# Kernel optimization log

Hardware: AMD Instinct MI355X
Metric: run time of the kernel (lower is better)

## Reference

```python
import jax, jax.numpy as jnp
import numpy as np

T, LQ, C = 6, 300, 256
NH, NL, PC, TW, PT = 8, 4, 4, 2, 2
DFF = 1024
HD = C // NH
SHAPES = [(96, 128), (48, 64), (24, 32), (12, 16)]
LIN = sum(h * w for h, w in SHAPES)
EPS = 1e-5


def _ln(x, g, b):
    m = x.mean(-1, keepdims=True)
    v = ((x - m) ** 2).mean(-1, keepdims=True)
    return (x - m) * jax.lax.rsqrt(v + EPS) * g + b


def _bilinear(img, loc):
    # img [T, Hl, Wl, NH, HD]; loc [T, Q, NH, P, 2] (x, y), normalized [0,1],
    # grid_sample align_corners=False + zero padding convention.
    Hl, Wl = img.shape[1], img.shape[2]
    x = loc[..., 0] * Wl - 0.5
    y = loc[..., 1] * Hl - 0.5
    x0f = jnp.floor(x)
    y0f = jnp.floor(y)
    wx = x - x0f
    wy = y - y0f
    x0 = x0f.astype(jnp.int32)
    y0 = y0f.astype(jnp.int32)
    flat = img.transpose(0, 3, 1, 2, 4).reshape(img.shape[0], NH, Hl * Wl, HD)
    b = jnp.arange(img.shape[0])[:, None, None, None]
    h = jnp.arange(NH)[None, :, None, None]

    def corner(yi, xi, w):
        valid = (xi >= 0) & (xi < Wl) & (yi >= 0) & (yi < Hl)
        idx = jnp.clip(yi, 0, Hl - 1) * Wl + jnp.clip(xi, 0, Wl - 1)
        g = flat[b, h, idx.transpose(0, 2, 1, 3)]  # [T, NH, Q, P, HD]
        w = jnp.where(valid, w, 0.0).transpose(0, 2, 1, 3)
        return g * w[..., None]

    out = (corner(y0, x0, (1 - wx) * (1 - wy)) + corner(y0, x0 + 1, wx * (1 - wy))
           + corner(y0 + 1, x0, (1 - wx) * wy) + corner(y0 + 1, x0 + 1, wx * wy))
    return out.transpose(0, 2, 1, 3, 4)  # [T, Q, NH, P, HD]


def _forward(tgt, query_pos, reference_points, curr_frame_offsets,
             other_frames_temporal_offsets, src, src_padding_mask,
             in_proj_w, in_proj_b, sa_out_w, sa_out_b,
             norm1_g, norm1_b, norm2_g, norm2_b, norm3_g, norm3_b,
             value_w, value_b, soff_w, soff_b, toff_w, toff_b,
             attn_w, attn_b, cross_out_w, cross_out_b,
             lin1_w, lin1_b, lin2_w, lin2_b):
    # ---- self attention (per-frame MHA over queries) ----
    q = tgt + query_pos
    wq, wk, wv = jnp.split(in_proj_w, 3, axis=0)
    bq, bk, bv = jnp.split(in_proj_b, 3)
    qh = ((q @ wq.T + bq) * (1.0 / np.sqrt(HD))).reshape(T, LQ, NH, HD)
    kh = (q @ wk.T + bk).reshape(T, LQ, NH, HD)
    vh = (tgt @ wv.T + bv).reshape(T, LQ, NH, HD)
    att = jax.nn.softmax(jnp.einsum('bqhd,bkhd->bhqk', qh, kh), axis=-1)
    sa = jnp.einsum('bhqk,bkhd->bqhd', att, vh).reshape(T, LQ, C) @ sa_out_w.T + sa_out_b
    tgt = _ln(tgt + sa, norm2_g, norm2_b)

    # ---- temporal multi-scale deformable cross attention ----
    qc = tgt + query_pos
    value = src @ value_w.T + value_b
    value = jnp.where(src_padding_mask[..., None], 0.0, value)
    value = value.reshape(T, LIN, NH, HD)

    soff = (qc @ soff_w.T + soff_b).reshape(T, LQ, NH, NL, PC, 2)
    toff = (qc @ toff_w.T + toff_b).reshape(T, LQ, NH, NL, TW, PT, 2)
    aw = (qc @ attn_w.T + attn_b).reshape(T, LQ, NH, NL * (PC + TW * PT))
    aw = jax.nn.softmax(aw, axis=-1).reshape(T, LQ, NH, NL, PC + TW * PT)
    aw_c = aw[..., :PC]                                  # [T,LQ,NH,NL,PC]
    aw_t = aw[..., PC:].reshape(T, LQ, NH, NL, TW, PT)

    norm = jnp.array([[w, h] for h, w in SHAPES], jnp.float32)  # [NL,2] (x,y)
    ref = reference_points[:, :, None, :, None, :]       # [T,LQ,1,NL,1,2]
    cfo = curr_frame_offsets[:, :, None, :, None, :]
    loc_c = ref + cfo + soff / norm[None, None, None, :, None, :]
    ofo = other_frames_temporal_offsets.transpose(0, 1, 3, 2, 4)[:, :, None, :, :, None, :]
    loc_t = ref[:, :, :, :, None, :, :] + ofo + toff / norm[None, None, None, :, None, None, :]

    # temporal window frame indices: nearest neighbours, clipped to clip bounds
    deltas = np.array([-(i // 2 + 1) if i % 2 == 0 else (i // 2 + 1) for i in range(TW)])
    frame_idx = np.clip(np.arange(T)[:, None] + deltas[None, :], 0, T - 1)  # [T,TW]

    out = jnp.zeros((T, LQ, NH, HD), tgt.dtype)
    start = 0
    for l, (hl, wl) in enumerate(SHAPES):
        v_l = value[:, start:start + hl * wl].reshape(T, hl, wl, NH, HD)
        s = _bilinear(v_l, loc_c[:, :, :, l])            # [T,LQ,NH,PC,HD]
        out = out + (s * aw_c[:, :, :, l, :, None]).sum(3)
        for w in range(TW):
            s = _bilinear(v_l[frame_idx[:, w]], loc_t[:, :, :, l, w])
            out = out + (s * aw_t[:, :, :, l, w, :, None]).sum(3)
        start += hl * wl
    cross = out.reshape(T, LQ, C) @ cross_out_w.T + cross_out_b
    tgt = _ln(tgt + cross, norm1_g, norm1_b)

    # ---- FFN ----
    ff = jax.nn.relu(tgt @ lin1_w.T + lin1_b) @ lin2_w.T + lin2_b
    return _ln(tgt + ff, norm3_g, norm3_b)


def setup_inputs():
    ks = jax.random.split(jax.random.key(0), 24)
    r = lambda i, s: jax.random.normal(ks[i], s, jnp.float32)
    u = lambda i, s: jax.random.uniform(ks[i], s, dtype=jnp.float32)
    w = lambda i, s: r(i, s) * 0.02
    shp = np.array(SHAPES, np.int64)
    lsi = np.concatenate([[0], np.cumsum(shp[:, 0] * shp[:, 1])[:-1]])
    return {
        'tgt': r(0, (T, LQ, C)),
        'query_pos': r(1, (T, LQ, C)),
        'reference_points': u(2, (T, LQ, NL, 2)),
        'curr_frame_offsets': u(3, (T, LQ, NL, 2)) * 0.1,
        'other_frames_temporal_offsets': u(4, (T, LQ, TW, NL, 2)) * 0.1,
        'src': r(5, (T, LIN, C)),
        'src_spatial_shapes': jnp.asarray(shp),
        'level_start_index': jnp.asarray(lsi),
        'src_padding_mask': jnp.zeros((T, LIN), bool),
        'in_proj_w': w(6, (3 * C, C)), 'in_proj_b': jnp.zeros((3 * C,)),
        'sa_out_w': w(7, (C, C)), 'sa_out_b': jnp.zeros((C,)),
        'norm1_g': jnp.ones((C,)), 'norm1_b': jnp.zeros((C,)),
        'norm2_g': jnp.ones((C,)), 'norm2_b': jnp.zeros((C,)),
        'norm3_g': jnp.ones((C,)), 'norm3_b': jnp.zeros((C,)),
        'value_w': w(8, (C, C)), 'value_b': jnp.zeros((C,)),
        'soff_w': w(9, (NH * NL * PC * 2, C)), 'soff_b': jnp.zeros((NH * NL * PC * 2,)),
        'toff_w': w(10, (NH * NL * TW * PT * 2, C)), 'toff_b': jnp.zeros((NH * NL * TW * PT * 2,)),
        'attn_w': w(11, (NH * NL * (PC + TW * PT), C)), 'attn_b': jnp.zeros((NH * NL * (PC + TW * PT),)),
        'cross_out_w': w(12, (C, C)), 'cross_out_b': jnp.zeros((C,)),
        'lin1_w': w(13, (DFF, C)), 'lin1_b': jnp.zeros((DFF,)),
        'lin2_w': w(14, (C, DFF)), 'lin2_b': jnp.zeros((C,)),
    }


def reference(tgt, query_pos, reference_points, curr_frame_offsets,
              other_frames_temporal_offsets, src, src_spatial_shapes,
              level_start_index, src_padding_mask,
              in_proj_w, in_proj_b, sa_out_w, sa_out_b,
              norm1_g, norm1_b, norm2_g, norm2_b, norm3_g, norm3_b,
              value_w, value_b, soff_w, soff_b, toff_w, toff_b,
              attn_w, attn_b, cross_out_w, cross_out_b,
              lin1_w, lin1_b, lin2_w, lin2_b):
    # src_spatial_shapes / level_start_index are static (match SHAPES constants)
    return _forward(tgt, query_pos, reference_points, curr_frame_offsets,
                    other_frames_temporal_offsets, src, src_padding_mask,
                    in_proj_w, in_proj_b, sa_out_w, sa_out_b,
                    norm1_g, norm1_b, norm2_g, norm2_b, norm3_g, norm3_b,
                    value_w, value_b, soff_w, soff_b, toff_w, toff_b,
                    attn_w, attn_b, cross_out_w, cross_out_b,
                    lin1_w, lin1_b, lin2_w, lin2_b)
```

## Files before the change

### kernel.cpp

```cpp
#include <hip/hip_runtime.h>
#include <math.h>

#define T_ 6
#define LQ_ 300
#define C_ 256
#define NH_ 8
#define HD_ 32
#define NL_ 4
#define PC_ 4
#define TW_ 2
#define PT_ 2
#define DFF_ 1024
#define LIN_ 16320
#define NQ_ (T_*LQ_)

typedef unsigned int uint32;
typedef unsigned short us;

__device__ __forceinline__ float b2f(us u) {
    union { float f; unsigned i; } x; x.i = ((unsigned)u) << 16; return x.f;
}
__device__ __forceinline__ us f2b(float f) {
    union { float f; unsigned i; } x; x.f = f;
    unsigned r = x.i + 0x7fffu + ((x.i >> 16) & 1u);
    return (us)(r >> 16);
}
__device__ __forceinline__ uint32 pack2(float a, float b) {
    return (uint32)f2b(a) | ((uint32)f2b(b) << 16);
}

typedef __bf16 bf16x8 __attribute__((ext_vector_type(8)));
typedef float  f32x4  __attribute__((ext_vector_type(4)));

__global__ void add_f32(const float4* __restrict__ a, const float4* __restrict__ b,
                        float4* __restrict__ o, int n4) {
    int i = blockIdx.x * 256 + threadIdx.x;
    if (i < n4) {
        float4 x = a[i], y = b[i];
        o[i] = make_float4(x.x + y.x, x.y + y.y, x.z + y.z, x.w + y.w);
    }
}

template<bool RELU>
__device__ __forceinline__ void gemm64_core(
        us* As, us* Bs,
        const float* __restrict__ A, const float* __restrict__ Bw,
        const float* __restrict__ bias, float* __restrict__ Cmat,
        int ldc, int cn0, int M, int K) {
    constexpr int LDA = 40;
    int tid  = threadIdx.x;
    int wave = tid >> 6, lane = tid & 63;
    int bm = blockIdx.x * 64;
    int wm = (wave >> 1) * 32, wn = (wave & 1) * 32;

    f32x4 acc00 = {0.f,0.f,0.f,0.f}, acc01 = {0.f,0.f,0.f,0.f};
    f32x4 acc10 = {0.f,0.f,0.f,0.f}, acc11 = {0.f,0.f,0.f,0.f};

    int srow = tid >> 2, scol = (tid & 3) * 8;
    int arow = bm + srow;
    const bool aval = arow < M;
    const size_t aoff = (size_t)arow * K + scol;
    const size_t boff = (size_t)srow * K + scol;

    int fr = lane & 15, quad = lane >> 4;
    const us* pa0 = As + (wm + fr) * LDA + quad * 8;
    const us* pa1 = pa0 + 16 * LDA;
    const us* pb0 = Bs + (wn + fr) * LDA + quad * 8;
    const us* pb1 = pb0 + 16 * LDA;

    for (int k0 = 0; k0 < K; k0 += 256) {
        float4 ar[8][2], br[8][2];
        #pragma unroll
        for (int c = 0; c < 8; ++c) {
            int kk = k0 + c * 32;
            if (aval) {
                ar[c][0] = *(const float4*)(A + aoff + kk);
                ar[c][1] = *(const float4*)(A + aoff + kk + 4);
            } else {
                ar[c][0] = make_float4(0.f,0.f,0.f,0.f);
                ar[c][1] = make_float4(0.f,0.f,0.f,0.f);
            }
            br[c][0] = *(const float4*)(Bw + boff + kk);
            br[c][1] = *(const float4*)(Bw + boff + kk + 4);
        }
        #pragma unroll
        for (int c = 0; c < 8; ++c) {
            uint4 ap, bp;
            ap.x = pack2(ar[c][0].x, ar[c][0].y); ap.y = pack2(ar[c][0].z, ar[c][0].w);
            ap.z = pack2(ar[c][1].x, ar[c][1].y); ap.w = pack2(ar[c][1].z, ar[c][1].w);
            bp.x = pack2(br[c][0].x, br[c][0].y); bp.y = pack2(br[c][0].z, br[c][0].w);
            bp.z = pack2(br[c][1].x, br[c][1].y); bp.w = pack2(br[c][1].z, br[c][1].w);
            __syncthreads();
            *(uint4*)(As + srow * LDA + scol) = ap;
            *(uint4*)(Bs + srow * LDA + scol) = bp;
            __syncthreads();
            bf16x8 a0 = *(const bf16x8*)pa0;
            bf16x8 a1 = *(const bf16x8*)pa1;
            bf16x8 b0 = *(const bf16x8*)pb0;
            bf16x8 b1 = *(const bf16x8*)pb1;
            acc00 = __builtin_amdgcn_mfma_f32_16x16x32_bf16(a0, b0, acc00, 0, 0, 0);
            acc01 = __builtin_amdgcn_mfma_f32_16x16x32_bf16(a0, b1, acc01, 0, 0, 0);
            acc10 = __builtin_amdgcn_mfma_f32_16x16x32_bf16(a1, b0, acc10, 0, 0, 0);
            acc11 = __builtin_amdgcn_mfma_f32_16x16x32_bf16(a1, b1, acc11, 0, 0, 0);
        }
    }

    int n0l = wn + fr, n1l = n0l + 16;
    float bias0 = bias[n0l], bias1 = bias[n1l];
    int mbase = bm + wm + quad * 4;
    #pragma unroll
    for (int r = 0; r < 4; ++r) {
        int m0 = mbase + r, m1 = m0 + 16;
        float v00 = acc00[r] + bias0, v01 = acc01[r] + bias1;
        float v10 = acc10[r] + bias0, v11 = acc11[r] + bias1;
        if (RELU) {
            v00 = fmaxf(v00, 0.f); v01 = fmaxf(v01, 0.f);
            v10 = fmaxf(v10, 0.f); v11 = fmaxf(v11, 0.f);
        }
        if (m0 < M) {
            Cmat[(size_t)m0 * ldc + cn0 + n0l] = v00;
            Cmat[(size_t)m0 * ldc + cn0 + n1l] = v01;
        }
        if (m1 < M) {
            Cmat[(size_t)m1 * ldc + cn0 + n0l] = v10;
            Cmat[(size_t)m1 * ldc + cn0 + n1l] = v11;
        }
    }
}

template<bool RELU>
__global__ __launch_bounds__(256, 2) void gemm_std(
        const float* __restrict__ A, const float* __restrict__ W,
        const float* __restrict__ bias, float* __restrict__ C,
        int M, int N, int K) {
    __shared__ __align__(16) us As[64 * 40];
    __shared__ __align__(16) us Bs[64 * 40];
    int cn0 = blockIdx.y * 64;
    gemm64_core<RELU>(As, Bs, A, W + (size_t)cn0 * K, bias + cn0, C, N, cn0, M, K);
}

__global__ __launch_bounds__(256, 2) void gemm_qkv(
        const float* __restrict__ qin, const float* __restrict__ tgt,
        const float* __restrict__ w, const float* __restrict__ b,
        float* __restrict__ qkb, float* __restrict__ vbuf) {
    __shared__ __align__(16) us As[64 * 40];
    __shared__ __align__(16) us Bs[64 * 40];
    int y = blockIdx.y;
    const float* A; const float* W; const float* bias; float* O; int ldc, cn0;
    if (y < 8) {
        A = qin; W = w + (size_t)y * 64 * 256; bias = b + y * 64;
        O = qkb; ldc = 512; cn0 = y * 64;
    } else {
        int yy = y - 8;
        A = tgt; W = w + (size_t)(512 + yy * 64) * 256; bias = b + 512 + yy * 64;
        O = vbuf; ldc = 256; cn0 = yy * 64;
    }
    gemm64_core<false>(As, Bs, A, W, bias, O, ldc, cn0, NQ_, 256);
}

__global__ __launch_bounds__(256, 2) void gemm_proj3(
        const float* __restrict__ qc,
        const float* __restrict__ sw, const float* __restrict__ sb,
        const float* __restrict__ tw, const float* __restrict__ tb,
        const float* __restrict__ aw, const float* __restrict__ ab,
        float* __restrict__ so, float* __restrict__ to, float* __restrict__ ao) {
    __shared__ __align__(16) us As[64 * 40];
    __shared__ __align__(16) us Bs[64 * 40];
    int y = blockIdx.y, g = y >> 2, cn0 = (y & 3) * 64;
    const float* W; const float* bias; float* O;
    if (g == 0)      { W = sw; bias = sb; O = so; }
    else if (g == 1) { W = tw; bias = tb; O = to; }
    else             { W = aw; bias = ab; O = ao; }
    gemm64_core<false>(As, Bs, qc, W + (size_t)cn0 * 256, bias + cn0, O, 256, cn0, NQ_, 256);
}

__global__ __launch_bounds__(256, 2) void gemm_value(
        const float* __restrict__ src, const float* __restrict__ W,
        const float* __restrict__ bias, us* __restrict__ out) {
    constexpr int LDA = 40;
    __shared__ __align__(16) us As[64 * LDA];
    __shared__ __align__(16) us Bs[256 * LDA];
    int tid = threadIdx.x, wave = tid >> 6, lane = tid & 63;
    int bm = blockIdx.x * 64;
    int fr = lane & 15, quad = lane >> 4;
    f32x4 acc[4][4];
    #pragma unroll
    for (int i = 0; i < 4; ++i)
        #pragma unroll
        for (int j = 0; j < 4; ++j) { f32x4 z = {0.f,0.f,0.f,0.f}; acc[i][j] = z; }

    for (int k0 = 0; k0 < 256; k0 += 32) {
        float4 av[2], bv[8];
        #pragma unroll
        for (int i = 0; i < 2; ++i) {
            int f = i * 256 + tid;
            av[i] = *(const float4*)(src + (size_t)(bm + (f >> 3)) * 256 + k0 + (f & 7) * 4);
        }
        #pragma unroll
        for (int i = 0; i < 8; ++i) {
            int f = i * 256 + tid;
            bv[i] = *(const float4*)(W + (size_t)(f >> 3) * 256 + k0 + (f & 7) * 4);
        }
        __syncthreads();
        #pragma unroll
        for (int i = 0; i < 2; ++i) {
            int f = i * 256 + tid;
            uint2 p; p.x = pack2(av[i].x, av[i].y); p.y = pack2(av[i].z, av[i].w);
            *(uint2*)(As + (f >> 3) * LDA + (f & 7) * 4) = p;
        }
        #pragma unroll
        for (int i = 0; i < 8; ++i) {
            int f = i * 256 + tid;
            uint2 p; p.x = pack2(bv[i].x, bv[i].y); p.y = pack2(bv[i].z, bv[i].w);
            *(uint2*)(Bs + (f >> 3) * LDA + (f & 7) * 4) = p;
        }
        __syncthreads();
        bf16x8 af[4], bfv[4];
        #pragma unroll
        for (int mt = 0; mt < 4; ++mt)
            af[mt] = *(const bf16x8*)(As + (mt * 16 + fr) * LDA + quad * 8);
        #pragma unroll
        for (int nt = 0; nt < 4; ++nt)
            bfv[nt] = *(const bf16x8*)(Bs + (wave * 64 + nt * 16 + fr) * LDA + quad * 8);
        #pragma unroll
        for (int mt = 0; mt < 4; ++mt)
            #pragma unroll
            for (int nt = 0; nt < 4; ++nt)
                acc[mt][nt] = __builtin_amdgcn_mfma_f32_16x16x32_bf16(af[mt], bfv[nt], acc[mt][nt], 0, 0, 0);
    }
    #pragma unroll
    for (int nt = 0; nt < 4; ++nt) {
        int n = wave * 64 + nt * 16 + fr;
        float bs = bias[n];
        #pragma unroll
        for (int mt = 0; mt < 4; ++mt) {
            int mbase = bm + mt * 16 + quad * 4;
            #pragma unroll
            for (int r = 0; r < 4; ++r)
                out[(size_t)(mbase + r) * 256 + n] = f2b(acc[mt][nt][r] + bs);
        }
    }
}

__global__ __launch_bounds__(256) void attn_kernel(
        const float* __restrict__ qk, const float* __restrict__ vb,
        float* __restrict__ sain) {
    __shared__ uint32 Ksu[300 * 17];
    __shared__ uint32 Vsu[300 * 17];
    __shared__ float  Qs[32 * 32];
    __shared__ float  ps[4][304];
    int t = blockIdx.x / NH_, h = blockIdx.x % NH_;
    int q0 = blockIdx.y * 32;
    int tid = threadIdx.x;

    for (int idx = tid; idx < 300 * 16; idx += 256) {
        int row = idx >> 4, cc = idx & 15;
        float2 kv = *(const float2*)(qk + (size_t)(t * 300 + row) * 512 + 256 + h * 32 + 2 * cc);
        float2 vv = *(const float2*)(vb + (size_t)(t * 300 + row) * 256 + h * 32 + 2 * cc);
        Ksu[row * 17 + cc] = pack2(kv.x, kv.y);
        Vsu[row * 17 + cc] = pack2(vv.x, vv.y);
    }
    for (int idx = tid; idx < 1024; idx += 256) {
        int row = idx >> 5, d = idx & 31;
        int q = q0 + row;
        Qs[idx] = (q < 300) ? qk[(size_t)(t * 300 + q) * 512 + h * 32 + d] : 0.f;
    }
    __syncthreads();

    int wavei = tid >> 6, lane = tid & 63;
    const float scale = 0.17677669529663687f;

    for (int i = 0; i < 8; ++i) {
        int q = q0 + wavei * 8 + i;
        int ql = wavei * 8 + i;
        float qv[32];
        #pragma unroll
        for (int d = 0; d < 32; ++d) qv[d] = Qs[ql * 32 + d];

        float sc[5], mx = -1e30f;
        #pragma unroll
        for (int m = 0; m < 5; ++m) {
            int k = lane + 64 * m;
            float s = -1e30f;
            if (k < 300) {
                s = 0.f;
                #pragma unroll
                for (int dd = 0; dd < 16; ++dd) {
                    uint32 u = Ksu[k * 17 + dd];
                    s += qv[2 * dd]     * b2f((us)u)
                       + qv[2 * dd + 1] * b2f((us)(u >> 16));
                }
                s *= scale;
            }
            sc[m] = s; mx = fmaxf(mx, s);
        }
        #pragma unroll
        for (int off = 1; off < 64; off <<= 1) mx = fmaxf(mx, __shfl_xor(mx, off));
        float sum = 0.f;
        #pragma unroll
        for (int m = 0; m < 5; ++m) {
            int k = lane + 64 * m;
            float ev = (k < 300) ? __expf(sc[m] - mx) : 0.f;
            if (k < 300) ps[wavei][k] = ev;
            sum += ev;
        }
        #pragma unroll
        for (int off = 1; off < 64; off <<= 1) sum += __shfl_xor(sum, off);
        float inv = 1.f / sum;
        __syncthreads();

        int e16 = lane & 15, kh = lane >> 4;
        float ox = 0.f, oy = 0.f;
        int kbeg = kh * 75;
        for (int k = kbeg; k < kbeg + 75; ++k) {
            float p = ps[wavei][k];
            uint32 u = Vsu[k * 17 + e16];
            ox += p * b2f((us)u);
            oy += p * b2f((us)(u >> 16));
        }
        ox += __shfl_xor(ox, 16); ox += __shfl_xor(ox, 32);
        oy += __shfl_xor(oy, 16); oy += __shfl_xor(oy, 32);
        if (q < 300 && kh == 0) {
            *(float2*)(sain + (size_t)(t * 300 + q) * 256 + h * 32 + 2 * e16)
                = make_float2(ox * inv, oy * inv);
        }
        __syncthreads();
    }
}

__global__ __launch_bounds__(256) void sample_kernel(
        const float* __restrict__ awl,   const float* __restrict__ refp,
        const float* __restrict__ cfo,   const float* __restrict__ ofo,
        const float* __restrict__ soffo, const float* __restrict__ toffo,
        const us* __restrict__ value, float* __restrict__ samp) {
    const int HL[4] = {96, 48, 24, 12};
    const int WL[4] = {128, 64, 32, 16};
    const int ST[4] = {0, 12288, 15360, 16128};
    int b = blockIdx.x;
    int t = b / LQ_;
    int tid = threadIdx.x, h = tid >> 5, d = tid & 31;
    size_t row = (size_t)b;

    float logit = awl[row * 256 + h * 32 + d];
    float mx = logit;
    #pragma unroll
    for (int off = 16; off >= 1; off >>= 1) mx = fmaxf(mx, __shfl_xor(mx, off, 32));
    float e = __expf(logit - mx);
    float s = e;
    #pragma unroll
    for (int off = 16; off >= 1; off >>= 1) s += __shfl_xor(s, off, 32);
    float myw = e / s;

    float acc = 0.f;
    for (int smp = 0; smp < 32; ++smp) {
        int l = smp >> 3, j = smp & 7;
        float wgt = __shfl(myw, smp, 32);
        int Hl = HL[l], Wl = WL[l], st = ST[l];
        float rx = refp[(row * 4 + l) * 2 + 0];
        float ry = refp[(row * 4 + l) * 2 + 1];
        float lx, ly; int frame;
        if (j < 4) {
            lx = rx + cfo[(row * 4 + l) * 2 + 0]
               + soffo[row * 256 + h * 32 + l * 8 + j * 2 + 0] / (float)Wl;
            ly = ry + cfo[(row * 4 + l) * 2 + 1]
               + soffo[row * 256 + h * 32 + l * 8 + j * 2 + 1] / (float)Hl;
            frame = t;
        } else {
            int wi = (j - 4) >> 1, p = (j - 4) & 1;
            lx = rx + ofo[((row * 2 + wi) * 4 + l) * 2 + 0]
               + toffo[row * 256 + h * 32 + l * 8 + wi * 4 + p * 2 + 0] / (float)Wl;
            ly = ry + ofo[((row * 2 + wi) * 4 + l) * 2 + 1]
               + toffo[row * 256 + h * 32 + l * 8 + wi * 4 + p * 2 + 1] / (float)Hl;
            frame = t + (wi == 0 ? -1 : 1);
            frame = frame < 0 ? 0 : (frame > T_ - 1 ? T_ - 1 : frame);
        }
        float x = lx * (float)Wl - 0.5f, y = ly * (float)Hl - 0.5f;
        float xf = floorf(x), yf = floorf(y);
        float wx = x - xf, wy = y - yf;
        int x0 = (int)xf, y0 = (int)yf;
        float sacc = 0.f;
        size_t base = ((size_t)frame * LIN_ + st) * 256 + h * 32 + d;
        #pragma unroll
        for (int cy = 0; cy < 2; ++cy) {
            int yi = y0 + cy;
            if (yi < 0 || yi >= Hl) continue;
            float wyv = cy ? wy : 1.f - wy;
            #pragma unroll
            for (int cx = 0; cx < 2; ++cx) {
                int xi = x0 + cx;
                if (xi < 0 || xi >= Wl) continue;
                float wv = wyv * (cx ? wx : 1.f - wx);
                sacc += wv * b2f(value[base + (size_t)(yi * Wl + xi) * 256]);
            }
        }
        acc += wgt * sacc;
    }
    samp[row * 256 + h * 32 + d] = acc;
}

__global__ __launch_bounds__(256) void ln_kernel(
        const float* __restrict__ x, const float* __restrict__ y,
        const float* __restrict__ g, const float* __restrict__ bb,
        float* __restrict__ out,
        const float* __restrict__ pos, float* __restrict__ out2) {
    int row = blockIdx.x, c = threadIdx.x;
    size_t idx = (size_t)row * 256 + c;
    float v = x[idx] + y[idx];
    float s = v;
    #pragma unroll
    for (int off = 1; off < 64; off <<= 1) s += __shfl_xor(s, off);
    __shared__ float red[4];
    int wv = c >> 6;
    if ((c & 63) == 0) red[wv] = s;
    __syncthreads();
    float mean = (red[0] + red[1] + red[2] + red[3]) * (1.0f / 256.0f);
    float dv = v - mean;
    float s2 = dv * dv;
    #pragma unroll
    for (int off = 1; off < 64; off <<= 1) s2 += __shfl_xor(s2, off);
    __syncthreads();
    if ((c & 63) == 0) red[wv] = s2;
    __syncthreads();
    float var = (red[0] + red[1] + red[2] + red[3]) * (1.0f / 256.0f);
    float o = dv * rsqrtf(var + 1e-5f) * g[c] + bb[c];
    out[idx] = o;
    if (out2) out2[idx] = o + pos[idx];
}

extern "C" void kernel_launch(void* const* d_in, const int* in_sizes, int n_in,
                              void* d_out, int out_size, void* d_ws, size_t ws_size,
                              hipStream_t stream) {
    (void)in_sizes; (void)n_in; (void)out_size; (void)ws_size;
    typedef const float* cfp;
    cfp tgt   = (cfp)d_in[0];
    cfp qpos  = (cfp)d_in[1];
    cfp refp  = (cfp)d_in[2];
    cfp cfo   = (cfp)d_in[3];
    cfp ofo   = (cfp)d_in[4];
    cfp src   = (cfp)d_in[5];
    cfp in_proj_w = (cfp)d_in[9];
    cfp in_proj_b = (cfp)d_in[10];
    cfp sa_out_w  = (cfp)d_in[11];
    cfp sa_out_b  = (cfp)d_in[12];
    cfp n1g = (cfp)d_in[13], n1b = (cfp)d_in[14];
    cfp n2g = (cfp)d_in[15], n2b = (cfp)d_in[16];
    cfp n3g = (cfp)d_in[17], n3b = (cfp)d_in[18];
    cfp value_w = (cfp)d_in[19], value_b = (cfp)d_in[20];
    cfp soff_w = (cfp)d_in[21], soff_b = (cfp)d_in[22];
    cfp toff_w = (cfp)d_in[23], toff_b = (cfp)d_in[24];
    cfp attn_w = (cfp)d_in[25], attn_b = (cfp)d_in[26];
    cfp cross_w = (cfp)d_in[27], cross_b = (cfp)d_in[28];
    cfp lin1_w = (cfp)d_in[29], lin1_b = (cfp)d_in[30];
    cfp lin2_w = (cfp)d_in[31], lin2_b = (cfp)d_in[32];

    char* wp = (char*)d_ws;
    const size_t ROWB = (size_t)NQ_ * 256 * 4;
    us* value = (us*)wp;  wp += (size_t)T_ * LIN_ * 256 * 2;
    float* bigreg = (float*)wp;  wp += 4 * ROWB;
    float* qin  = bigreg;
    float* qkb  = bigreg + (size_t)NQ_ * 256;
    float* vbuf = bigreg + (size_t)NQ_ * 768;
    float* ff1  = bigreg;
    float* sain   = (float*)wp; wp += ROWB;   float* awl    = sain;
    float* sap    = (float*)wp; wp += ROWB;   float* soffo  = sap;
    float* tgt2   = (float*)wp; wp += ROWB;   float* ff2    = tgt2;
    float* qc     = (float*)wp; wp += ROWB;   float* samp   = qc;
    float* toffo  = (float*)wp; wp += ROWB;
    float* crossp = (float*)wp; wp += ROWB;
    float* tgt3   = (float*)wp; wp += ROWB;

    dim3 blk(256);
    const int mb = (NQ_ + 63) / 64;

    add_f32<<<dim3((NQ_ * 64 + 255) / 256), blk, 0, stream>>>(
        (const float4*)tgt, (const float4*)qpos, (float4*)qin, NQ_ * 64);
    gemm_qkv<<<dim3(mb, 12), blk, 0, stream>>>(qin, tgt, in_proj_w, in_proj_b, qkb, vbuf);
    attn_kernel<<<dim3(T_ * NH_, 10), blk, 0, stream>>>(qkb, vbuf, sain);
    gemm_std<false><<<dim3(mb, 4), blk, 0, stream>>>(sain, sa_out_w, sa_out_b, sap, NQ_, 256, 256);
    ln_kernel<<<dim3(NQ_), blk, 0, stream>>>(tgt, sap, n2g, n2b, tgt2, qpos, qc);
    gemm_proj3<<<dim3(mb, 12), blk, 0, stream>>>(qc, soff_w, soff_b, toff_w, toff_b,
                                                 attn_w, attn_b, soffo, toffo, awl);
    gemm_value<<<dim3((T_ * LIN_) / 64), blk, 0, stream>>>(src, value_w, value_b, value);
    sample_kernel<<<dim3(NQ_), blk, 0, stream>>>(awl, refp, cfo, ofo, soffo, toffo, value, samp);
    gemm_std<false><<<dim3(mb, 4), blk, 0, stream>>>(samp, cross_w, cross_b, crossp, NQ_, 256, 256);
    ln_kernel<<<dim3(NQ_), blk, 0, stream>>>(tgt2, crossp, n1g, n1b, tgt3, nullptr, nullptr);
    gemm_std<true><<<dim3(mb, 16), blk, 0, stream>>>(tgt3, lin1_w, lin1_b, ff1, NQ_, 1024, 256);
    gemm_std<false><<<dim3(mb, 4), blk, 0, stream>>>(ff1, lin2_w, lin2_b, ff2, NQ_, 256, 1024);
    ln_kernel<<<dim3(NQ_), blk, 0, stream>>>(tgt3, ff2, n3g, n3b, (float*)d_out, nullptr, nullptr);
}
```

Baseline: 404.9 us.

## Fuse residual+LayerNorm into full-width GEMMs and fold pos-add into QKV GEMM

Replaces the three out-projection GEMM + separate LayerNorm kernel pairs with one full-row (N=256) GEMM kernel that adds bias and residual, computes mean/variance per row via shuffles and shared memory, and writes the normalized output. It also folds the tgt+query_pos addition into the QKV GEMM's A-load, and adds register prefetching of the next K chunk in the full GEMM. The value GEMM moves first and pack2 uses the hardware bf16 conversion. This removes several launches and intermediate round trips. The cost is fewer blocks (mb=29 only) for the fused GEMMs, lower parallelism, and single-pass variance with slightly different numerics.

```diff
diff --git a/kernel.cpp b/kernel.cpp
--- a/kernel.cpp
+++ b/kernel.cpp
@@ -1,4 +1,5 @@
 #include <hip/hip_runtime.h>
+#include <hip/hip_bf16.h>
 #include <math.h>
 
 #define T_ 6
@@ -26,25 +27,19 @@
     return (us)(r >> 16);
 }
 __device__ __forceinline__ uint32 pack2(float a, float b) {
-    return (uint32)f2b(a) | ((uint32)f2b(b) << 16);
+    union { __hip_bfloat162 h; uint32 u; } c;
+    c.h = __float22bfloat162_rn(make_float2(a, b));
+    return c.u;
 }
 
 typedef __bf16 bf16x8 __attribute__((ext_vector_type(8)));
 typedef float  f32x4  __attribute__((ext_vector_type(4)));
-
-__global__ void add_f32(const float4* __restrict__ a, const float4* __restrict__ b,
-                        float4* __restrict__ o, int n4) {
-    int i = blockIdx.x * 256 + threadIdx.x;
-    if (i < n4) {
-        float4 x = a[i], y = b[i];
-        o[i] = make_float4(x.x + y.x, x.y + y.y, x.z + y.z, x.w + y.w);
-    }
-}
 
 template<bool RELU>
 __device__ __forceinline__ void gemm64_core(
         us* As, us* Bs,
-        const float* __restrict__ A, const float* __restrict__ Bw,
+        const float* __restrict__ A, const float* __restrict__ A2,
+        const float* __restrict__ Bw,
         const float* __restrict__ bias, float* __restrict__ Cmat,
         int ldc, int cn0, int M, int K) {
     constexpr int LDA = 40;
@@ -76,6 +71,12 @@
             if (aval) {
                 ar[c][0] = *(const float4*)(A + aoff + kk);
                 ar[c][1] = *(const float4*)(A + aoff + kk + 4);
+                if (A2) {
+                    float4 p0 = *(const float4*)(A2 + aoff + kk);
+                    float4 p1 = *(const float4*)(A2 + aoff + kk + 4);
+                    ar[c][0].x += p0.x; ar[c][0].y += p0.y; ar[c][0].z += p0.z; ar[c][0].w += p0.w;
+                    ar[c][1].x += p1.x; ar[c][1].y += p1.y; ar[c][1].z += p1.z; ar[c][1].w += p1.w;
+                }
             } else {
                 ar[c][0] = make_float4(0.f,0.f,0.f,0.f);
                 ar[c][1] = make_float4(0.f,0.f,0.f,0.f);
@@ -136,26 +137,24 @@
     __shared__ __align__(16) us As[64 * 40];
     __shared__ __align__(16) us Bs[64 * 40];
     int cn0 = blockIdx.y * 64;
-    gemm64_core<RELU>(As, Bs, A, W + (size_t)cn0 * K, bias + cn0, C, N, cn0, M, K);
+    gemm64_core<RELU>(As, Bs, A, nullptr, W + (size_t)cn0 * K, bias + cn0, C, N, cn0, M, K);
 }
 
 __global__ __launch_bounds__(256, 2) void gemm_qkv(
-        const float* __restrict__ qin, const float* __restrict__ tgt,
+        const float* __restrict__ tgt, const float* __restrict__ qpos,
         const float* __restrict__ w, const float* __restrict__ b,
         float* __restrict__ qkb, float* __restrict__ vbuf) {
     __shared__ __align__(16) us As[64 * 40];
     __shared__ __align__(16) us Bs[64 * 40];
     int y = blockIdx.y;
-    const float* A; const float* W; const float* bias; float* O; int ldc, cn0;
     if (y < 8) {
-        A = qin; W = w + (size_t)y * 64 * 256; bias = b + y * 64;
-        O = qkb; ldc = 512; cn0 = y * 64;
+        gemm64_core<false>(As, Bs, tgt, qpos, w + (size_t)y * 64 * 256, b + y * 64,
+                           qkb, 512, y * 64, NQ_, 256);
     } else {
         int yy = y - 8;
-        A = tgt; W = w + (size_t)(512 + yy * 64) * 256; bias = b + 512 + yy * 64;
-        O = vbuf; ldc = 256; cn0 = yy * 64;
-    }
-    gemm64_core<false>(As, Bs, A, W, bias, O, ldc, cn0, NQ_, 256);
+        gemm64_core<false>(As, Bs, tgt, nullptr, w + (size_t)(512 + yy * 64) * 256,
+                           b + 512 + yy * 64, vbuf, 256, yy * 64, NQ_, 256);
+    }
 }
 
 __global__ __launch_bounds__(256, 2) void gemm_proj3(
@@ -171,37 +170,57 @@
     if (g == 0)      { W = sw; bias = sb; O = so; }
     else if (g == 1) { W = tw; bias = tb; O = to; }
     else             { W = aw; bias = ab; O = ao; }
-    gemm64_core<false>(As, Bs, qc, W + (size_t)cn0 * 256, bias + cn0, O, 256, cn0, NQ_, 256);
-}
-
-__global__ __launch_bounds__(256, 2) void gemm_value(
-        const float* __restrict__ src, const float* __restrict__ W,
-        const float* __restrict__ bias, us* __restrict__ out) {
+    gemm64_core<false>(As, Bs, qc, nullptr, W + (size_t)cn0 * 256, bias + cn0, O, 256, cn0, NQ_, 256);
+}
+
+template<int MODE>
+__global__ __launch_bounds__(256, 2) void gemm_full(
+        const float* __restrict__ A, const float* __restrict__ W,
+        const float* __restrict__ bias, int M, int K,
+        us* __restrict__ out_bf,
+        const float* __restrict__ resid, const float* __restrict__ lng,
+        const float* __restrict__ lnb, float* __restrict__ out_ln,
+        const float* __restrict__ pos, float* __restrict__ out2) {
     constexpr int LDA = 40;
     __shared__ __align__(16) us As[64 * LDA];
     __shared__ __align__(16) us Bs[256 * LDA];
+    __shared__ float lred[2][64][4];
+    __shared__ float lmv[2][64];
     int tid = threadIdx.x, wave = tid >> 6, lane = tid & 63;
     int bm = blockIdx.x * 64;
     int fr = lane & 15, quad = lane >> 4;
+
     f32x4 acc[4][4];
     #pragma unroll
     for (int i = 0; i < 4; ++i)
         #pragma unroll
         for (int j = 0; j < 4; ++j) { f32x4 z = {0.f,0.f,0.f,0.f}; acc[i][j] = z; }
 
-    for (int k0 = 0; k0 < 256; k0 += 32) {
-        float4 av[2], bv[8];
+    const int KC = K >> 5;
+    float4 av[2], bv[8];
+
+    auto ldA = [&](int c) {
+        int k0 = c * 32;
         #pragma unroll
         for (int i = 0; i < 2; ++i) {
             int f = i * 256 + tid;
-            av[i] = *(const float4*)(src + (size_t)(bm + (f >> 3)) * 256 + k0 + (f & 7) * 4);
-        }
+            int r = bm + (f >> 3);
+            if (r < M) av[i] = *(const float4*)(A + (size_t)r * K + k0 + (f & 7) * 4);
+            else       av[i] = make_float4(0.f, 0.f, 0.f, 0.f);
+        }
+    };
+    auto ldB = [&](int c) {
+        int k0 = c * 32;
         #pragma unroll
         for (int i = 0; i < 8; ++i) {
             int f = i * 256 + tid;
-            bv[i] = *(const float4*)(W + (size_t)(f >> 3) * 256 + k0 + (f & 7) * 4);
-        }
-        __syncthreads();
+            bv[i] = *(const float4*)(W + (size_t)(f >> 3) * K + k0 + (f & 7) * 4);
+        }
+    };
+
+    ldA(0); ldB(0);
+    for (int c = 0; c < KC; ++c) {
+        if (c) __syncthreads();
         #pragma unroll
         for (int i = 0; i < 2; ++i) {
             int f = i * 256 + tid;
@@ -215,6 +234,7 @@
             *(uint2*)(Bs + (f >> 3) * LDA + (f & 7) * 4) = p;
         }
         __syncthreads();
+        if (c + 1 < KC) { ldA(c + 1); ldB(c + 1); }
         bf16x8 af[4], bfv[4];
         #pragma unroll
         for (int mt = 0; mt < 4; ++mt)
@@ -228,16 +248,88 @@
             for (int nt = 0; nt < 4; ++nt)
                 acc[mt][nt] = __builtin_amdgcn_mfma_f32_16x16x32_bf16(af[mt], bfv[nt], acc[mt][nt], 0, 0, 0);
     }
-    #pragma unroll
-    for (int nt = 0; nt < 4; ++nt) {
-        int n = wave * 64 + nt * 16 + fr;
-        float bs = bias[n];
+
+    if (MODE == 0) {
+        #pragma unroll
+        for (int nt = 0; nt < 4; ++nt) {
+            int n = wave * 64 + nt * 16 + fr;
+            float bs = bias[n];
+            #pragma unroll
+            for (int mt = 0; mt < 4; ++mt) {
+                int mbase = bm + mt * 16 + quad * 4;
+                #pragma unroll
+                for (int r = 0; r < 4; ++r) {
+                    int m = mbase + r;
+                    if (m < M) out_bf[(size_t)m * 256 + n] = f2b(acc[mt][nt][r] + bs);
+                }
+            }
+        }
+    } else {
+        int col[4]; float bcol[4];
+        #pragma unroll
+        for (int nt = 0; nt < 4; ++nt) {
+            col[nt] = wave * 64 + nt * 16 + fr;
+            bcol[nt] = bias[col[nt]];
+        }
         #pragma unroll
         for (int mt = 0; mt < 4; ++mt) {
-            int mbase = bm + mt * 16 + quad * 4;
             #pragma unroll
-            for (int r = 0; r < 4; ++r)
-                out[(size_t)(mbase + r) * 256 + n] = f2b(acc[mt][nt][r] + bs);
+            for (int r = 0; r < 4; ++r) {
+                int m = bm + mt * 16 + quad * 4 + r;
+                #pragma unroll
+                for (int nt = 0; nt < 4; ++nt) {
+                    float rv = (m < M) ? resid[(size_t)m * 256 + col[nt]] : 0.f;
+                    acc[mt][nt][r] += bcol[nt] + rv;
+                }
+            }
+        }
+        #pragma unroll
+        for (int mt = 0; mt < 4; ++mt) {
+            #pragma unroll
+            for (int r = 0; r < 4; ++r) {
+                float s  = acc[mt][0][r] + acc[mt][1][r] + acc[mt][2][r] + acc[mt][3][r];
+                float s2 = acc[mt][0][r]*acc[mt][0][r] + acc[mt][1][r]*acc[mt][1][r]
+                         + acc[mt][2][r]*acc[mt][2][r] + acc[mt][3][r]*acc[mt][3][r];
+                #pragma unroll
+                for (int off = 1; off < 16; off <<= 1) {
+                    s  += __shfl_xor(s,  off);
+                    s2 += __shfl_xor(s2, off);
+                }
+                if (fr == 0) {
+                    int row = mt * 16 + quad * 4 + r;
+                    lred[0][row][wave] = s;
+                    lred[1][row][wave] = s2;
+                }
+            }
+        }
+        __syncthreads();
+        if (tid < 64) {
+            float s  = lred[0][tid][0] + lred[0][tid][1] + lred[0][tid][2] + lred[0][tid][3];
+            float s2 = lred[1][tid][0] + lred[1][tid][1] + lred[1][tid][2] + lred[1][tid][3];
+            float mean = s * (1.0f / 256.0f);
+            float var  = s2 * (1.0f / 256.0f) - mean * mean;
+            lmv[0][tid] = mean;
+            lmv[1][tid] = rsqrtf(var + 1e-5f);
+        }
+        __syncthreads();
+        float gcol[4], b2col[4];
+        #pragma unroll
+        for (int nt = 0; nt < 4; ++nt) { gcol[nt] = lng[col[nt]]; b2col[nt] = lnb[col[nt]]; }
+        #pragma unroll
+        for (int mt = 0; mt < 4; ++mt) {
+            #pragma unroll
+            for (int r = 0; r < 4; ++r) {
+                int row = mt * 16 + quad * 4 + r;
+                int m = bm + row;
+                if (m >= M) continue;
+                float mean = lmv[0][row], rstd = lmv[1][row];
+                #pragma unroll
+                for (int nt = 0; nt < 4; ++nt) {
+                    float o = (acc[mt][nt][r] - mean) * rstd * gcol[nt] + b2col[nt];
+                    out_ln[(size_t)m * 256 + col[nt]] = o;
+                    if (pos) out2[(size_t)m * 256 + col[nt]] = o + pos[(size_t)m * 256 + col[nt]];
+                }
+            }
         }
     }
 }
@@ -396,35 +488,6 @@
         acc += wgt * sacc;
     }
     samp[row * 256 + h * 32 + d] = acc;
-}
-
-__global__ __launch_bounds__(256) void ln_kernel(
-        const float* __restrict__ x, const float* __restrict__ y,
-        const float* __restrict__ g, const float* __restrict__ bb,
-        float* __restrict__ out,
-        const float* __restrict__ pos, float* __restrict__ out2) {
-    int row = blockIdx.x, c = threadIdx.x;
-    size_t idx = (size_t)row * 256 + c;
-    float v = x[idx] + y[idx];
-    float s = v;
-    #pragma unroll
-    for (int off = 1; off < 64; off <<= 1) s += __shfl_xor(s, off);
-    __shared__ float red[4];
-    int wv = c >> 6;
-    if ((c & 63) == 0) red[wv] = s;
-    __syncthreads();
-    float mean = (red[0] + red[1] + red[2] + red[3]) * (1.0f / 256.0f);
-    float dv = v - mean;
-    float s2 = dv * dv;
-    #pragma unroll
-    for (int off = 1; off < 64; off <<= 1) s2 += __shfl_xor(s2, off);
-    __syncthreads();
-    if ((c & 63) == 0) red[wv] = s2;
-    __syncthreads();
-    float var = (red[0] + red[1] + red[2] + red[3]) * (1.0f / 256.0f);
-    float o = dv * rsqrtf(var + 1e-5f) * g[c] + bb[c];
-    out[idx] = o;
-    if (out2) out2[idx] = o + pos[idx];
 }
 
 extern "C" void kernel_launch(void* const* d_in, const int* in_sizes, int n_in,
@@ -457,34 +520,36 @@
     const size_t ROWB = (size_t)NQ_ * 256 * 4;
     us* value = (us*)wp;  wp += (size_t)T_ * LIN_ * 256 * 2;
     float* bigreg = (float*)wp;  wp += 4 * ROWB;
-    float* qin  = bigreg;
-    float* qkb  = bigreg + (size_t)NQ_ * 256;
-    float* vbuf = bigreg + (size_t)NQ_ * 768;
+    float* qkb  = bigreg;
+    float* vbuf = bigreg + (size_t)NQ_ * 512;
     float* ff1  = bigreg;
     float* sain   = (float*)wp; wp += ROWB;   float* awl    = sain;
     float* sap    = (float*)wp; wp += ROWB;   float* soffo  = sap;
-    float* tgt2   = (float*)wp; wp += ROWB;   float* ff2    = tgt2;
+    float* tgt2   = (float*)wp; wp += ROWB;
     float* qc     = (float*)wp; wp += ROWB;   float* samp   = qc;
     float* toffo  = (float*)wp; wp += ROWB;
-    float* crossp = (float*)wp; wp += ROWB;
     float* tgt3   = (float*)wp; wp += ROWB;
+    (void)sap;
 
     dim3 blk(256);
     const int mb = (NQ_ + 63) / 64;
 
-    add_f32<<<dim3((NQ_ * 64 + 255) / 256), blk, 0, stream>>>(
-        (const float4*)tgt, (const float4*)qpos, (float4*)qin, NQ_ * 64);
-    gemm_qkv<<<dim3(mb, 12), blk, 0, stream>>>(qin, tgt, in_proj_w, in_proj_b, qkb, vbuf);
+    gemm_full<0><<<dim3((T_ * LIN_) / 64), blk, 0, stream>>>(
+        src, value_w, value_b, T_ * LIN_, 256, value,
+        nullptr, nullptr, nullptr, nullptr, nullptr, nullptr);
+    gemm_qkv<<<dim3(mb, 12), blk, 0, stream>>>(tgt, qpos, in_proj_w, in_proj_b, qkb, vbuf);
     attn_kernel<<<dim3(T_ * NH_, 10), blk, 0, stream>>>(qkb, vbuf, sain);
-    gemm_std<false><<<dim3(mb, 4), blk, 0, stream>>>(sain, sa_out_w, sa_out_b, sap, NQ_, 256, 256);
-    ln_kernel<<<dim3(NQ_), blk, 0, stream>>>(tgt, sap, n2g, n2b, tgt2, qpos, qc);
+    gemm_full<1><<<dim3(mb), blk, 0, stream>>>(
+        sain, sa_out_w, sa_out_b, NQ_, 256, nullptr,
+        tgt, n2g, n2b, tgt2, qpos, qc);
     gemm_proj3<<<dim3(mb, 12), blk, 0, stream>>>(qc, soff_w, soff_b, toff_w, toff_b,
                                                  attn_w, attn_b, soffo, toffo, awl);
-    gemm_value<<<dim3((T_ * LIN_) / 64), blk, 0, stream>>>(src, value_w, value_b, value);
     sample_kernel<<<dim3(NQ_), blk, 0, stream>>>(awl, refp, cfo, ofo, soffo, toffo, value, samp);
-    gemm_std<false><<<dim3(mb, 4), blk, 0, stream>>>(samp, cross_w, cross_b, crossp, NQ_, 256, 256);
-    ln_kernel<<<dim3(NQ_), blk, 0, stream>>>(tgt2, crossp, n1g, n1b, tgt3, nullptr, nullptr);
+    gemm_full<1><<<dim3(mb), blk, 0, stream>>>(
+        samp, cross_w, cross_b, NQ_, 256, nullptr,
+        tgt2, n1g, n1b, tgt3, nullptr, nullptr);
     gemm_std<true><<<dim3(mb, 16), blk, 0, stream>>>(tgt3, lin1_w, lin1_b, ff1, NQ_, 1024, 256);
-    gemm_std<false><<<dim3(mb, 4), blk, 0, stream>>>(ff1, lin2_w, lin2_b, ff2, NQ_, 256, 1024);
-    ln_kernel<<<dim3(NQ_), blk, 0, stream>>>(tgt3, ff2, n3g, n3b, (float*)d_out, nullptr, nullptr);
-}
+    gemm_full<1><<<dim3(mb), blk, 0, stream>>>(
+        ff1, lin2_w, lin2_b, NQ_, 1024, nullptr,
+        tgt3, n3g, n3b, (float*)d_out, nullptr, nullptr);
+}
```

Measured after the change: 461.5 us. 14.0% more time.
